# Optimization experiments

Hardware: AMD Instinct MI355X
Metric: run time of the kernel (lower is better)

Reference implementation:

```python
import jax, jax.numpy as jnp
import numpy as np

WIN_H = 3
WIN_W = 3
DILATION = 1
CUT = 0.0  # module hard-codes self.cut = 0
EPS = 1e-12  # torch F.normalize eps


def _l2norm(x):
    # L2-normalize over channel dim (dim=1), matching torch.nn.functional.normalize
    n = jnp.sqrt(jnp.sum(x * x, axis=1, keepdims=True))
    return x / jnp.maximum(n, EPS)


def setup_inputs() -> dict:
    key = jax.random.key(0)
    k1, k2 = jax.random.split(key)
    B, C, H, W = 4, 128, 192, 256
    image = jax.random.normal(k1, (B, C, H, W), dtype=jnp.float32)
    event = jax.random.normal(k2, (B, C, H, W), dtype=jnp.float32)
    return {"image": image, "event": event}


def reference(image, event):
    B, C, H, W = image.shape
    img = _l2norm(image)
    evt = _l2norm(event)
    p = DILATION
    imgp = jnp.pad(img, ((0, 0), (0, 0), (p, p), (p, p)))
    evtp = jnp.pad(evt, ((0, 0), (0, 0), (p, p), (p, p)))
    # Unfold ordering: reshape(B, C, K, H, W) with K positions row-major over (i, j).
    # affinity_k(p) = sum_c img_shift_k(p) * evt_shift_k(p)  -> avoid im2col blowup,
    # compute per-offset shifted dot products instead.
    affs = []
    for i in range(WIN_H):
        for j in range(WIN_W):
            oi, oj = i * DILATION, j * DILATION
            a = jnp.sum(
                imgp[:, :, oi:oi + H, oj:oj + W] * evtp[:, :, oi:oi + H, oj:oj + W],
                axis=1,
            )  # [B, H, W]
            affs.append(a)
    affinity = jnp.stack(affs, axis=1)  # [B, K=9, H, W]
    # affinity[affinity < cut] = cut  with cut == 0
    return jnp.maximum(affinity, CUT)
```

## Files before the change

kernel.cpp:

```cpp
#include <hip/hip_runtime.h>

#define BB 4
#define CC 128
#define HH 192
#define WW 256
#define HW (HH * WW)

__global__ __launch_bounds__(256) void dotscatter_kernel(
    const float* __restrict__ img, const float* __restrict__ evt,
    float* __restrict__ out)
{
    const int blk = blockIdx.x;
    const int tid = threadIdx.x;
    const int qx  = tid & 15;
    const int cz  = tid >> 4;
    const int seg = blk & 3;
    const int row = blk >> 2;
    const int b   = row / HH;
    const int h   = row - b * HH;
    const int w0  = seg * 64 + (qx << 2);
    const int base0 = b * CC * HW + h * WW + w0;
    const int cbase = cz * 8;

    float4 aii = make_float4(0.f, 0.f, 0.f, 0.f);
    float4 aee = make_float4(0.f, 0.f, 0.f, 0.f);
    float4 aie = make_float4(0.f, 0.f, 0.f, 0.f);

    #pragma unroll
    for (int c = 0; c < 8; ++c) {
        const float4 iv = *reinterpret_cast<const float4*>(img + base0 + (cbase + c) * HW);
        const float4 ev = *reinterpret_cast<const float4*>(evt + base0 + (cbase + c) * HW);
        aii.x += iv.x * iv.x; aii.y += iv.y * iv.y; aii.z += iv.z * iv.z; aii.w += iv.w * iv.w;
        aee.x += ev.x * ev.x; aee.y += ev.y * ev.y; aee.z += ev.z * ev.z; aee.w += ev.w * ev.w;
        aie.x += iv.x * ev.x; aie.y += iv.y * ev.y; aie.z += iv.z * ev.z; aie.w += iv.w * ev.w;
    }

    __shared__ float s_ii[16][64];
    __shared__ float s_ee[16][64];
    __shared__ float s_ie[16][64];
    const int p4 = qx << 2;
    s_ii[cz][p4 + 0] = aii.x; s_ii[cz][p4 + 1] = aii.y; s_ii[cz][p4 + 2] = aii.z; s_ii[cz][p4 + 3] = aii.w;
    s_ee[cz][p4 + 0] = aee.x; s_ee[cz][p4 + 1] = aee.y; s_ee[cz][p4 + 2] = aee.z; s_ee[cz][p4 + 3] = aee.w;
    s_ie[cz][p4 + 0] = aie.x; s_ie[cz][p4 + 1] = aie.y; s_ie[cz][p4 + 2] = aie.z; s_ie[cz][p4 + 3] = aie.w;
    __syncthreads();

    if (tid < 64) {
        float ii = 0.f, ee = 0.f, ie = 0.f;
        #pragma unroll
        for (int k = 0; k < 16; ++k) {
            ii += s_ii[k][tid];
            ee += s_ee[k][tid];
            ie += s_ie[k][tid];
        }
        const float ni = fmaxf(sqrtf(ii), 1e-12f);
        const float ne = fmaxf(sqrtf(ee), 1e-12f);
        const float dc = fmaxf(ie / (ni * ne), 0.0f);

        const int w  = seg * 64 + tid;
        const int ob = b * 9;
        #pragma unroll
        for (int i = 0; i < 3; ++i) {
            const int th = h + 1 - i;
            if (th < 0 || th >= HH) continue;
            #pragma unroll
            for (int j = 0; j < 3; ++j) {
                const int tw = w + 1 - j;
                if (tw >= 0 && tw < WW) {
                    __builtin_nontemporal_store(
                        dc, out + (((ob + i * 3 + j) * HH + th) * WW + tw));
                }
            }
        }
    }
}

extern "C" void kernel_launch(void* const* d_in, const int* in_sizes, int n_in,
                              void* d_out, int out_size, void* d_ws, size_t ws_size,
                              hipStream_t stream) {
    const float* img = (const float*)d_in[0];
    const float* evt = (const float*)d_in[1];
    float* out = (float*)d_out;

    hipMemsetAsync(out, 0, (size_t)out_size * sizeof(float), stream);

    dotscatter_kernel<<<BB * HH * 4, 256, 0, stream>>>(img, evt, out);
}
```

Measured before the change: 41.96 us.

## Fuse border zeroing into kernel and write full output rows with vector stores

Drops the separate memset of the output and has each block handle a full image row with 512 threads. The per-pixel cosine values are staged in shared memory and each of the 9 offset planes is written as coalesced float4 rows. Rows and columns that fall outside the image are written as explicit zeros. This removes the extra memset pass and the scattered scalar stores, in exchange for an additional barrier and fewer, larger blocks.

```diff
diff --git a/kernel.cpp b/kernel.cpp
--- a/kernel.cpp
+++ b/kernel.cpp
@@ -6,70 +6,91 @@
 #define WW 256
 #define HW (HH * WW)
 
-__global__ __launch_bounds__(256) void dotscatter_kernel(
+typedef float floatx4 __attribute__((ext_vector_type(4)));
+
+__global__ __launch_bounds__(512) void fused_kernel(
     const float* __restrict__ img, const float* __restrict__ evt,
     float* __restrict__ out)
 {
-    const int blk = blockIdx.x;
+    const int row = blockIdx.x;
     const int tid = threadIdx.x;
-    const int qx  = tid & 15;
-    const int cz  = tid >> 4;
-    const int seg = blk & 3;
-    const int row = blk >> 2;
+    const int qx  = tid & 63;
+    const int cz  = tid >> 6;
     const int b   = row / HH;
     const int h   = row - b * HH;
-    const int w0  = seg * 64 + (qx << 2);
-    const int base0 = b * CC * HW + h * WW + w0;
-    const int cbase = cz * 8;
+    const int base0 = b * CC * HW + h * WW + (qx << 2);
 
-    float4 aii = make_float4(0.f, 0.f, 0.f, 0.f);
-    float4 aee = make_float4(0.f, 0.f, 0.f, 0.f);
-    float4 aie = make_float4(0.f, 0.f, 0.f, 0.f);
+    const float* ip = img + base0 + (cz * 16) * HW;
+    const float* ep = evt + base0 + (cz * 16) * HW;
 
+    floatx4 aii = 0.f, aee = 0.f, aie = 0.f;
     #pragma unroll
-    for (int c = 0; c < 8; ++c) {
-        const float4 iv = *reinterpret_cast<const float4*>(img + base0 + (cbase + c) * HW);
-        const float4 ev = *reinterpret_cast<const float4*>(evt + base0 + (cbase + c) * HW);
-        aii.x += iv.x * iv.x; aii.y += iv.y * iv.y; aii.z += iv.z * iv.z; aii.w += iv.w * iv.w;
-        aee.x += ev.x * ev.x; aee.y += ev.y * ev.y; aee.z += ev.z * ev.z; aee.w += ev.w * ev.w;
-        aie.x += iv.x * ev.x; aie.y += iv.y * ev.y; aie.z += iv.z * ev.z; aie.w += iv.w * ev.w;
+    for (int c = 0; c < 16; ++c) {
+        const floatx4 iv = *reinterpret_cast<const floatx4*>(ip + c * HW);
+        const floatx4 ev = *reinterpret_cast<const floatx4*>(ep + c * HW);
+        aii += iv * iv;
+        aee += ev * ev;
+        aie += iv * ev;
     }
 
-    __shared__ float s_ii[16][64];
-    __shared__ float s_ee[16][64];
-    __shared__ float s_ie[16][64];
+    __shared__ float s_ii[8][256];
+    __shared__ float s_ee[8][256];
+    __shared__ float s_ie[8][256];
+    __shared__ float s_dc[256];
     const int p4 = qx << 2;
     s_ii[cz][p4 + 0] = aii.x; s_ii[cz][p4 + 1] = aii.y; s_ii[cz][p4 + 2] = aii.z; s_ii[cz][p4 + 3] = aii.w;
     s_ee[cz][p4 + 0] = aee.x; s_ee[cz][p4 + 1] = aee.y; s_ee[cz][p4 + 2] = aee.z; s_ee[cz][p4 + 3] = aee.w;
     s_ie[cz][p4 + 0] = aie.x; s_ie[cz][p4 + 1] = aie.y; s_ie[cz][p4 + 2] = aie.z; s_ie[cz][p4 + 3] = aie.w;
     __syncthreads();
 
-    if (tid < 64) {
+    if (tid < 256) {
         float ii = 0.f, ee = 0.f, ie = 0.f;
         #pragma unroll
-        for (int k = 0; k < 16; ++k) {
+        for (int k = 0; k < 8; ++k) {
             ii += s_ii[k][tid];
             ee += s_ee[k][tid];
             ie += s_ie[k][tid];
         }
         const float ni = fmaxf(sqrtf(ii), 1e-12f);
         const float ne = fmaxf(sqrtf(ee), 1e-12f);
-        const float dc = fmaxf(ie / (ni * ne), 0.0f);
+        s_dc[tid] = fmaxf(ie / (ni * ne), 0.0f);
+    }
+    __syncthreads();
 
-        const int w  = seg * 64 + tid;
-        const int ob = b * 9;
+    const size_t obase = (size_t)b * 9 * HH * WW;
+    for (int q = tid; q < 576; q += 512) {
+        const int p  = q >> 6;
+        const int i  = p / 3;
+        const int j  = p - 3 * i;
+        const int th = h + 1 - i;
+        if (th < 0 || th >= HH) continue;
+        const int c0 = (q & 63) << 2;
+        float t[4];
         #pragma unroll
-        for (int i = 0; i < 3; ++i) {
-            const int th = h + 1 - i;
-            if (th < 0 || th >= HH) continue;
-            #pragma unroll
-            for (int j = 0; j < 3; ++j) {
-                const int tw = w + 1 - j;
-                if (tw >= 0 && tw < WW) {
-                    __builtin_nontemporal_store(
-                        dc, out + (((ob + i * 3 + j) * HH + th) * WW + tw));
-                }
-            }
+        for (int e = 0; e < 4; ++e) {
+            const int sc = c0 + e + j - 1;
+            t[e] = (sc >= 0 && sc < WW) ? s_dc[sc] : 0.0f;
+        }
+        floatx4 v = {t[0], t[1], t[2], t[3]};
+        __builtin_nontemporal_store(
+            v, reinterpret_cast<floatx4*>(out + obase + ((size_t)p * HH + th) * WW + c0));
+    }
+    if (h == 0) {
+        const floatx4 z = 0.f;
+        for (int q = tid; q < 192; q += 512) {
+            const int p  = q >> 6;
+            const int c0 = (q & 63) << 2;
+            __builtin_nontemporal_store(
+                z, reinterpret_cast<floatx4*>(out + obase + (size_t)p * HH * WW + c0));
+        }
+    }
+    if (h == HH - 1) {
+        const floatx4 z = 0.f;
+        for (int q = tid; q < 192; q += 512) {
+            const int p  = 6 + (q >> 6);
+            const int c0 = (q & 63) << 2;
+            __builtin_nontemporal_store(
+                z, reinterpret_cast<floatx4*>(out + obase + ((size_t)p * HH + (HH - 1)) * WW + c0));
         }
     }
 }
@@ -81,7 +102,5 @@
     const float* evt = (const float*)d_in[1];
     float* out = (float*)d_out;
 
-    hipMemsetAsync(out, 0, (size_t)out_size * sizeof(float), stream);
-
-    dotscatter_kernel<<<BB * HH * 4, 256, 0, stream>>>(img, evt, out);
+    fused_kernel<<<BB * HH, 512, 0, stream>>>(img, evt, out);
 }
```

Result: faster. 34.99 us (-16.6%).
